# Performance work log

Measured on AMD Instinct MI355X. Metric: run time of the kernel, lower is better.

Reference implementation:

```python
import jax, jax.numpy as jnp
import numpy as np

B, L, D_MODEL = 2, 4096, 1024
D_STATE, D_CONV, EXPAND, HEADDIM = 128, 4, 2, 64
D_INNER = EXPAND * D_MODEL              # 2048
NHEADS = D_INNER // HEADDIM             # 32
CONV_DIM = D_INNER + 2 * D_STATE        # 2304 (ngroups=1)
D_IN_PROJ = 2 * D_INNER + 2 * D_STATE + NHEADS  # 4384
CHUNK = 128
EPS = 1e-5


def _segsum(a):
    # a: (..., T) log-decays -> (..., T, T) lower-triangular segment sums, -inf above diagonal
    T = a.shape[-1]
    cs = jnp.cumsum(a, axis=-1)
    seg = cs[..., :, None] - cs[..., None, :]
    mask = jnp.tril(jnp.ones((T, T), dtype=bool))
    return jnp.where(mask, seg, -jnp.inf)


def _forward(x, norm_w, norm_b, in_proj_w, conv_w, conv_b, dt_bias, A_log, D, rms_w, out_proj_w):
    b, l, _ = x.shape
    # pre-LayerNorm
    mu = jnp.mean(x, -1, keepdims=True)
    var = jnp.mean(jnp.square(x - mu), -1, keepdims=True)
    xn = (x - mu) * jax.lax.rsqrt(var + EPS) * norm_w + norm_b
    zxbcdt = xn @ in_proj_w.T                              # (b,l,D_IN_PROJ)
    z = zxbcdt[..., :D_INNER]
    xBC = zxbcdt[..., D_INNER:D_INNER + CONV_DIM]
    dt = jax.nn.softplus(zxbcdt[..., -NHEADS:] + dt_bias)  # (b,l,h)
    # causal depthwise conv1d + SiLU over (x, B, C)
    xc = jnp.pad(xBC.transpose(0, 2, 1), ((0, 0), (0, 0), (D_CONV - 1, 0)))
    xc = jax.lax.conv_general_dilated(xc, conv_w[:, None, :], (1,), 'VALID',
                                      feature_group_count=CONV_DIM,
                                      dimension_numbers=('NCH', 'OIH', 'NCH'))
    xBC = jax.nn.silu(xc + conv_b[None, :, None]).transpose(0, 2, 1)
    xs = xBC[..., :D_INNER].reshape(b, l, NHEADS, HEADDIM)
    Bm = xBC[..., D_INNER:D_INNER + D_STATE]               # (b,l,n)
    Cm = xBC[..., D_INNER + D_STATE:]                      # (b,l,n)
    # SSD chunked selective scan
    A = -jnp.exp(A_log)                                    # (h,)
    a = dt * A                                             # (b,l,h) log decay
    X = xs * dt[..., None]                                 # (b,l,h,p)
    c = l // CHUNK
    a_c = a.reshape(b, c, CHUNK, NHEADS).transpose(0, 3, 1, 2)   # (b,h,c,s)
    a_cum = jnp.cumsum(a_c, -1)
    Lmat = jnp.exp(_segsum(a_c))                           # (b,h,c,s,s)
    Xc = X.reshape(b, c, CHUNK, NHEADS, HEADDIM)
    Bc = Bm.reshape(b, c, CHUNK, D_STATE)
    Cc = Cm.reshape(b, c, CHUNK, D_STATE)
    # intra-chunk (diagonal block) output
    Y_diag = jnp.einsum('bcln,bcsn,bhcls,bcshp->bclhp', Cc, Bc, Lmat, Xc)
    # chunk-final states
    decay_states = jnp.exp(a_cum[..., -1:] - a_cum)        # (b,h,c,s)
    states = jnp.einsum('bcln,bhcl,bclhp->bchpn', Bc, decay_states, Xc)
    states = jnp.concatenate([jnp.zeros_like(states[:, :1]), states], axis=1)
    chunk_decay = jnp.exp(_segsum(jnp.pad(a_cum[..., -1], ((0, 0), (0, 0), (1, 0)))))  # (b,h,c+1,c+1)
    prev = jnp.einsum('bhzc,bchpn->bzhpn', chunk_decay, states)[:, :-1]  # (b,c,h,p,n)
    # inter-chunk (off-diagonal) output
    Y_off = jnp.einsum('bcln,bchpn,bhcl->bclhp', Cc, prev, jnp.exp(a_cum))
    y = (Y_diag + Y_off).reshape(b, l, NHEADS, HEADDIM) + D[None, None, :, None] * xs
    y = y.reshape(b, l, D_INNER)
    # gated RMSNorm (norm_before_gate=False): norm(y * silu(z))
    y = y * jax.nn.silu(z)
    y = y * jax.lax.rsqrt(jnp.mean(jnp.square(y), -1, keepdims=True) + EPS) * rms_w
    return x + y @ out_proj_w.T


def setup_inputs() -> dict:
    key = jax.random.key(0)
    ks = jax.random.split(key, 8)
    return {
        'x': jax.random.normal(ks[0], (B, L, D_MODEL), jnp.float32),
        'norm_w': jnp.ones((D_MODEL,), jnp.float32),
        'norm_b': jnp.zeros((D_MODEL,), jnp.float32),
        'in_proj_w': 0.02 * jax.random.normal(ks[1], (D_IN_PROJ, D_MODEL), jnp.float32),
        'conv_w': 0.2 * jax.random.normal(ks[2], (CONV_DIM, D_CONV), jnp.float32),
        'conv_b': jnp.zeros((CONV_DIM,), jnp.float32),
        'dt_bias': jax.random.uniform(ks[3], (NHEADS,), jnp.float32, -4.0, 0.0),
        'A_log': jnp.log(jax.random.uniform(ks[4], (NHEADS,), jnp.float32, 1.0, 16.0)),
        'D': jnp.ones((NHEADS,), jnp.float32),
        'rms_w': jnp.ones((D_INNER,), jnp.float32),
        'out_proj_w': 0.02 * jax.random.normal(ks[5], (D_MODEL, D_INNER), jnp.float32),
    }


def reference(x, norm_w, norm_b, in_proj_w, conv_w, conv_b, dt_bias, A_log, D, rms_w, out_proj_w):
    return _forward(x, norm_w, norm_b, in_proj_w, conv_w, conv_b, dt_bias, A_log, D, rms_w, out_proj_w)
```

## Files before the change

### kernel.cpp

```cpp
#include <hip/hip_runtime.h>

#define B_ 2
#define L_ 4096
#define DMODEL 1024
#define DSTATE 128
#define DINNER 2048
#define NH 32
#define HD 64
#define DPROJ 4384
#define DPROJP 4480
#define NC 32
#define EPSF 1e-5f
#define ROWS (B_*L_)

typedef unsigned short u16;
typedef __attribute__((ext_vector_type(8))) short s8v;
typedef __attribute__((ext_vector_type(4))) float f4v;
typedef __attribute__((ext_vector_type(4))) int i4v;
typedef __attribute__((ext_vector_type(2))) int i2v;
typedef __attribute__((ext_vector_type(4))) float fl4;

static __device__ __forceinline__ float b2f(u16 u){
  unsigned int x = ((unsigned int)u) << 16;
  return __builtin_bit_cast(float, x);
}
static __device__ __forceinline__ u16 f2b(float f){
  unsigned int x = __builtin_bit_cast(unsigned int, f);
  unsigned int r = x + 0x7FFFu + ((x >> 16) & 1u);
  return (u16)(r >> 16);
}
static __device__ __forceinline__ float softplusf(float x){
  return (x > 20.f) ? x : log1pf(expf(x));
}
static __device__ __forceinline__ void gl_lds16(const u16* g, u16* l){
  __builtin_amdgcn_global_load_lds(
    (const __attribute__((address_space(1))) unsigned int*)g,
    (__attribute__((address_space(3))) unsigned int*)l, 16, 0, 0);
}
static __device__ __forceinline__ int swz(int row, int col){
  return row*128 + ((((col >> 3) ^ (row & 15)) << 3) | (col & 7));
}
static __device__ __forceinline__ int swz64(int row, int col){
  return row*64 + ((((col >> 3) ^ (row & 7)) << 3) | (col & 7));
}
static __device__ __forceinline__ int osw(int t, int j){
  return t*64 + ((((j >> 3) ^ ((t >> 3) & 7)) << 3) | (j & 7));
}

__global__ void k_dbg(float* out, float v){ out[0] = v; }

#define NW1 ((size_t)DPROJP*DMODEL)
#define NW2 ((size_t)DMODEL*DINNER)
__global__ __launch_bounds__(256) void k_pack(const float* __restrict__ W1, const float* __restrict__ W2,
                                              u16* __restrict__ W1b, u16* __restrict__ W2b){
  size_t i = (size_t)blockIdx.x*256 + threadIdx.x;
  if (i < NW1){
    size_t n = i / DMODEL;
    W1b[i] = (n < DPROJ) ? f2b(W1[i]) : (u16)0;
  } else if (i < NW1 + NW2){
    size_t j = i - NW1;
    W2b[j] = f2b(W2[j]);
  }
}

__global__ __launch_bounds__(256) void k_ln(const float* __restrict__ x, const float* __restrict__ nw,
                                            const float* __restrict__ nb, u16* __restrict__ xn){
  int m = blockIdx.x; int tid = threadIdx.x;
  const float* row = x + (size_t)m*DMODEL;
  fl4 v = *(const fl4*)&row[tid*4];
  float s1 = v[0]+v[1]+v[2]+v[3];
  float s2 = v[0]*v[0]+v[1]*v[1]+v[2]*v[2]+v[3]*v[3];
  #pragma unroll
  for (int o=32;o;o>>=1){ s1 += __shfl_down(s1,o); s2 += __shfl_down(s2,o); }
  __shared__ float r1[4], r2[4];
  if ((tid&63)==0){ r1[tid>>6]=s1; r2[tid>>6]=s2; }
  __syncthreads();
  s1 = r1[0]+r1[1]+r1[2]+r1[3]; s2 = r2[0]+r2[1]+r2[2]+r2[3];
  float mu = s1 * (1.f/DMODEL);
  float var = s2 * (1.f/DMODEL) - mu*mu;
  float rs = rsqrtf(var + EPSF);
  u16* o = xn + (size_t)m*DMODEL + tid*4;
  #pragma unroll
  for (int k=0;k<4;k++)
    o[k] = f2b((v[k]-mu)*rs*nw[tid*4+k] + nb[tid*4+k]);
}

__global__ __launch_bounds__(256) void k_gemm_in(const u16* __restrict__ A, const u16* __restrict__ Bw,
                  u16* __restrict__ Cout, int K, int lda, int ldb, int ldc){
  __shared__ u16 smem[2*128*64];
  u16* sA = smem;
  u16* sB = smem + 128*64;
  int tid = threadIdx.x;
  int ln = tid & 63, wid = tid >> 6;
  int wr = wid >> 1, wc = wid & 1;
  size_t m0 = (size_t)blockIdx.x * 128, n0 = (size_t)blockIdx.y * 128;
  int lrow = ln >> 3;
  f4v acc[4][4] = {};
  for (int k0 = 0; k0 < K; k0 += 64){
    #pragma unroll
    for (int i = 0; i < 4; ++i){
      int seg = wid*4 + i;
      int row = seg*8 + lrow;
      int scol = ((ln & 7) ^ (row & 7)) * 8;
      gl_lds16(&A [(m0+row)*lda + k0 + scol], &sA[seg*512]);
      gl_lds16(&Bw[(n0+row)*ldb + k0 + scol], &sB[seg*512]);
    }
    __syncthreads();
    #pragma unroll
    for (int kk=0; kk<2; kk++){
      s8v af[4], bfr[4];
      #pragma unroll
      for (int t=0;t<4;t++){
        int col = kk*32 + (ln>>4)*8;
        af[t]  = *(const s8v*)&sA[swz64(wr*64+t*16+(ln&15), col)];
        bfr[t] = *(const s8v*)&sB[swz64(wc*64+t*16+(ln&15), col)];
      }
      #pragma unroll
      for (int mt=0;mt<4;mt++)
        #pragma unroll
        for (int nt=0;nt<4;nt++)
          acc[mt][nt] = __builtin_amdgcn_mfma_f32_16x16x32_bf16(af[mt], bfr[nt], acc[mt][nt], 0,0,0);
    }
    __syncthreads();
  }
  #pragma unroll
  for (int mt=0;mt<4;mt++)
    #pragma unroll
    for (int nt=0;nt<4;nt++)
      #pragma unroll
      for (int j=0;j<4;j++){
        int m = wr*64 + mt*16 + (ln>>4)*4 + j;
        int n = wc*64 + nt*16 + (ln&15);
        smem[m*128 + n] = f2b(acc[mt][nt][j]);
      }
  __syncthreads();
  #pragma unroll
  for (int it = 0; it < 8; ++it){
    int idx = (tid + it*256)*8;
    int row = idx >> 7, col = idx & 127;
    *(i4v*)&Cout[(m0+row)*ldc + n0 + col] = *(const i4v*)&smem[idx];
  }
}

__global__ __launch_bounds__(256) void k_gemm_out(const u16* __restrict__ A, const u16* __restrict__ Bw,
                  float* __restrict__ Cout, const float* __restrict__ resid,
                  int K, int lda, int ldb, int ldc){
  __shared__ u16 sA[128*64];
  __shared__ u16 sB[128*64];
  int tid = threadIdx.x;
  int ln = tid & 63, wid = tid >> 6;
  int wr = wid >> 1, wc = wid & 1;
  size_t m0 = (size_t)blockIdx.x * 128, n0 = (size_t)blockIdx.y * 128;
  int lrow = ln >> 3;
  f4v acc[4][4] = {};
  for (int k0 = 0; k0 < K; k0 += 64){
    #pragma unroll
    for (int i = 0; i < 4; ++i){
      int seg = wid*4 + i;
      int row = seg*8 + lrow;
      int scol = ((ln & 7) ^ (row & 7)) * 8;
      gl_lds16(&A [(m0+row)*lda + k0 + scol], &sA[seg*512]);
      gl_lds16(&Bw[(n0+row)*ldb + k0 + scol], &sB[seg*512]);
    }
    __syncthreads();
    #pragma unroll
    for (int kk=0; kk<2; kk++){
      s8v af[4], bfr[4];
      #pragma unroll
      for (int t=0;t<4;t++){
        int col = kk*32 + (ln>>4)*8;
        af[t]  = *(const s8v*)&sA[swz64(wr*64+t*16+(ln&15), col)];
        bfr[t] = *(const s8v*)&sB[swz64(wc*64+t*16+(ln&15), col)];
      }
      #pragma unroll
      for (int mt=0;mt<4;mt++)
        #pragma unroll
        for (int nt=0;nt<4;nt++)
          acc[mt][nt] = __builtin_amdgcn_mfma_f32_16x16x32_bf16(af[mt], bfr[nt], acc[mt][nt], 0,0,0);
    }
    __syncthreads();
  }
  #pragma unroll
  for (int mt=0;mt<4;mt++)
    #pragma unroll
    for (int nt=0;nt<4;nt++)
      #pragma unroll
      for (int j=0;j<4;j++){
        size_t m = m0 + wr*64 + mt*16 + (ln>>4)*4 + j;
        size_t n = n0 + wc*64 + nt*16 + (ln&15);
        Cout[m*ldc + n] = acc[mt][nt][j] + resid[m*ldc + n];
      }
}

__global__ __launch_bounds__(256) void k_conv(const u16* __restrict__ zx, const float* __restrict__ cw,
    const float* __restrict__ cb, const float* __restrict__ dtb, const float* __restrict__ A_log,
    u16* __restrict__ Xt, u16* __restrict__ Bln, u16* __restrict__ Bt,
    u16* __restrict__ Cln, float* __restrict__ dtg, float* __restrict__ acum){
  __shared__ u16 in_s[131*64];
  __shared__ u16 out_s[128*64];
  __shared__ float dt_s[128];
  __shared__ float a_s[128];
  int bid = blockIdx.x;
  int g = bid % 36;
  int c = (bid / 36) & 31;
  int b = bid / (36*32);
  int tid = threadIdx.x;
  int t0 = c*128;
  size_t rowb = (size_t)b*L_ + t0;
  for (int i8 = tid; i8 < 1048; i8 += 256){
    int r = i8 >> 3, j0 = (i8 & 7)*8;
    int t = t0 - 3 + r;
    i4v v;
    if (t >= 0) v = *(const i4v*)&zx[((size_t)b*L_ + t)*DPROJP + 2048 + g*64 + j0];
    else { v[0]=0; v[1]=0; v[2]=0; v[3]=0; }
    *(i4v*)&in_s[r*64 + j0] = v;
  }
  if (tid < 128){
    if (g < 32){
      float raw = b2f(zx[(rowb + tid)*DPROJP + (DPROJ - NH) + g]);
      float d = softplusf(raw + dtb[g]);
      dt_s[tid] = d;
      dtg[(size_t)(b*NH + g)*L_ + t0 + tid] = d;
      a_s[tid] = d * (-expf(A_log[g]));
    } else {
      dt_s[tid] = 0.f;
      a_s[tid] = 0.f;
    }
  }
  __syncthreads();
  #pragma unroll
  for (int d = 1; d < 128; d <<= 1){
    float v = 0.f;
    if (tid < 128 && tid >= d) v = a_s[tid - d];
    __syncthreads();
    if (tid < 128) a_s[tid] += v;
    __syncthreads();
  }
  if (g < 32 && tid < 128)
    acum[((size_t)((b*NH + g)*NC + c))*128 + tid] = a_s[tid];
  {
    int j = tid & 63;
    int ch = g*64 + j;
    float w0 = cw[ch*4+0], w1 = cw[ch*4+1], w2 = cw[ch*4+2], w3 = cw[ch*4+3];
    float bia = cb[ch];
    int tb = tid >> 6;
    #pragma unroll
    for (int it = 0; it < 32; ++it){
      int t = tb + it*4;
      float a = bia
        + w0*b2f(in_s[(t+0)*64 + j]) + w1*b2f(in_s[(t+1)*64 + j])
        + w2*b2f(in_s[(t+2)*64 + j]) + w3*b2f(in_s[(t+3)*64 + j]);
      out_s[osw(t, j)] = f2b(a / (1.f + __expf(-a)));
    }
  }
  __syncthreads();
  if (g < 32){
    for (int i = tid; i < 1024; i += 256){
      int j = i >> 4, tb = (i & 15)*8;
      i4v o; u16* ou = (u16*)&o;
      #pragma unroll
      for (int k = 0; k < 8; ++k)
        ou[k] = f2b(b2f(out_s[osw(tb + k, j)]) * dt_s[tb + k]);
      *(i4v*)&Xt[((size_t)((b*NH + g)*HD + j))*L_ + t0 + tb] = o;
    }
  } else {
    int q = g - 32;
    for (int i = tid; i < 1024; i += 256){
      int t = i >> 3, j0 = (i & 7)*8;
      i4v v = *(const i4v*)&out_s[osw(t, j0)];
      if (q < 2) *(i4v*)&Bln[(rowb + t)*DSTATE + q*64 + j0] = v;
      else       *(i4v*)&Cln[(rowb + t)*DSTATE + (q-2)*64 + j0] = v;
    }
    if (q < 2){
      for (int i = tid; i < 1024; i += 256){
        int j = i >> 4, tb = (i & 15)*8;
        i4v o; u16* ou = (u16*)&o;
        #pragma unroll
        for (int k = 0; k < 8; ++k) ou[k] = out_s[osw(tb + k, j)];
        *(i4v*)&Bt[((size_t)(b*DSTATE + q*64 + j))*L_ + t0 + tb] = o;
      }
    }
  }
}

__global__ __launch_bounds__(256) void k_states(const u16* __restrict__ Xt, const u16* __restrict__ Bt,
    const float* __restrict__ acum, u16* __restrict__ states){
  __shared__ u16 sX[64*128];
  __shared__ u16 sB[128*128];
  __shared__ float dec[128];
  int bid = blockIdx.x;
  int hg = bid & 7, c = (bid >> 3) & 31, b = bid >> 8;
  int tid = threadIdx.x;
  int ln = tid & 63, wid = tid >> 6;
  int wr = wid >> 1, wc = wid & 1;
  const u16* btb = Bt + (size_t)(b*DSTATE)*L_ + c*128;
  for (int i = tid*8; i < 128*128; i += 256*8){
    int n = i >> 7, l0 = i & 127;
    *(i4v*)&sB[swz(n, l0)] = *(const i4v*)&btb[(size_t)n*L_ + l0];
  }
  for (int hh = 0; hh < 4; ++hh){
    int h = hg*4 + hh;
    const float* acg = acum + ((size_t)((b*NH + h)*NC + c))*128;
    if (tid < 128) dec[tid] = __expf(acg[127] - acg[tid]);
    __syncthreads();
    const u16* xtb = Xt + ((size_t)((b*NH + h)*HD))*L_ + c*128;
    for (int i = tid*8; i < 64*128; i += 256*8){
      int p = i >> 7, l0 = i & 127;
      i4v v = *(const i4v*)&xtb[(size_t)p*L_ + l0];
      const u16* vu = (const u16*)&v;
      i4v o; u16* ou = (u16*)&o;
      #pragma unroll
      for (int j = 0; j < 8; ++j) ou[j] = f2b(b2f(vu[j]) * dec[l0 + j]);
      *(i4v*)&sX[swz(p, l0)] = o;
    }
    __syncthreads();
    f4v acc[2][4] = {};
    #pragma unroll
    for (int kk = 0; kk < 4; ++kk){
      s8v af[2], bfr[4];
      int col = kk*32 + (ln>>4)*8;
      #pragma unroll
      for (int t = 0; t < 2; ++t)
        af[t] = *(const s8v*)&sX[swz(wr*32 + t*16 + (ln&15), col)];
      #pragma unroll
      for (int t = 0; t < 4; ++t)
        bfr[t] = *(const s8v*)&sB[swz(wc*64 + t*16 + (ln&15), col)];
      #pragma unroll
      for (int mt = 0; mt < 2; ++mt)
        #pragma unroll
        for (int nt = 0; nt < 4; ++nt)
          acc[mt][nt] = __builtin_amdgcn_mfma_f32_16x16x32_bf16(af[mt], bfr[nt], acc[mt][nt], 0,0,0);
    }
    u16* out = states + ((size_t)((b*NC + c)*NH + h))*(HD*DSTATE);
    #pragma unroll
    for (int mt = 0; mt < 2; ++mt)
      #pragma unroll
      for (int nt = 0; nt < 4; ++nt){
        int n = wc*64 + nt*16 + (ln&15);
        #pragma unroll
        for (int j = 0; j < 4; ++j){
          int p = wr*32 + mt*16 + (ln>>4)*4 + j;
          out[(size_t)p*DSTATE + n] = f2b(acc[mt][nt][j]);
        }
      }
  }
}

__global__ __launch_bounds__(256) void k_scan(u16* __restrict__ states, const float* __restrict__ acum){
  int bid = blockIdx.x;
  int eb = bid & 7;
  int hb = bid >> 3;
  int h = hb & 31, b = hb >> 5;
  int tid = threadIdx.x;
  size_t ebase = (size_t)eb*1024 + (size_t)tid*4;
  size_t hoff = ((size_t)(b*NC*NH + h))*(HD*DSTATE) + ebase;
  float dec[NC];
  #pragma unroll
  for (int c = 0; c < NC; ++c)
    dec[c] = __expf(acum[((size_t)((b*NH + h)*NC + c))*128 + 127]);
  i2v w[NC];
  #pragma unroll
  for (int c = 0; c < NC; ++c)
    w[c] = *(const i2v*)&states[(size_t)c*(NH*HD*DSTATE) + hoff];
  float run[4] = {0.f, 0.f, 0.f, 0.f};
  #pragma unroll
  for (int c = 0; c < NC; ++c){
    u16* wu = (u16*)&w[c];
    #pragma unroll
    for (int j = 0; j < 4; ++j){
      float tmp = b2f(wu[j]);
      wu[j] = f2b(run[j]);
      run[j] = run[j]*dec[c] + tmp;
    }
  }
  #pragma unroll
  for (int c = 0; c < NC; ++c)
    *(i2v*)&states[(size_t)c*(NH*HD*DSTATE) + hoff] = w[c];
}

__global__ __launch_bounds__(256) void k_y(const u16* __restrict__ Cln, const u16* __restrict__ Bln,
    const u16* __restrict__ Xt, const u16* __restrict__ prev, const float* __restrict__ acum,
    const float* __restrict__ dtg, const float* __restrict__ Dp, u16* __restrict__ Y){
  __shared__ u16 sC[128*128];
  __shared__ u16 sBS[128*128];
  __shared__ float dt_s[128];
  int bid = blockIdx.x;
  int h = bid & 31, c = (bid >> 5) & 31, b = bid >> 10;
  int tid = threadIdx.x;
  size_t rowb = (size_t)b*L_ + c*128;
  const float* acg = acum + ((size_t)((b*NH + h)*NC + c))*128;
  if (tid < 128) dt_s[tid] = dtg[(size_t)(b*NH + h)*L_ + c*128 + tid];
  for (int i = tid*8; i < 128*128; i += 256*8){
    int row = i >> 7, col = i & 127;
    int d = swz(row, col);
    *(i4v*)&sC[d]  = *(const i4v*)&Cln[(rowb + row)*DSTATE + col];
    *(i4v*)&sBS[d] = *(const i4v*)&Bln[(rowb + row)*DSTATE + col];
  }
  __syncthreads();
  int ln = tid & 63, wid = tid >> 6;
  int wr = wid >> 1, wc = wid & 1;
  float Dh = Dp[h];
  f4v aS[4][4] = {};
  #pragma unroll
  for (int kk = 0; kk < 4; ++kk){
    s8v af[4], bfr[4];
    #pragma unroll
    for (int t = 0; t < 4; ++t){
      int col = kk*32 + (ln>>4)*8;
      af[t]  = *(const s8v*)&sC [swz(wr*64 + t*16 + (ln&15), col)];
      bfr[t] = *(const s8v*)&sBS[swz(wc*64 + t*16 + (ln&15), col)];
    }
    #pragma unroll
    for (int mt = 0; mt < 4; ++mt)
      #pragma unroll
      for (int nt = 0; nt < 4; ++nt)
        aS[mt][nt] = __builtin_amdgcn_mfma_f32_16x16x32_bf16(af[mt], bfr[nt], aS[mt][nt], 0,0,0);
  }
  __syncthreads();
  #pragma unroll
  for (int mt = 0; mt < 4; ++mt)
    #pragma unroll
    for (int nt = 0; nt < 4; ++nt){
      int s = wc*64 + nt*16 + (ln&15);
      float as = acg[s];
      #pragma unroll
      for (int j = 0; j < 4; ++j){
        int l = wr*64 + mt*16 + (ln>>4)*4 + j;
        float v = 0.f;
        if (s <= l){
          v = aS[mt][nt][j] * __expf(acg[l] - as);
          if (s == l) v += Dh / dt_s[l];
        }
        sBS[swz(l, s)] = f2b(v);
      }
    }
  __syncthreads();
  const u16* xtb = Xt + ((size_t)((b*NH + h)*HD))*L_ + c*128;
  const u16* pv = prev + ((size_t)((b*NC + c)*NH + h))*(HD*DSTATE);
  f4v aD[4][2] = {}, aO[4][2] = {};
  #pragma unroll
  for (int kk = 0; kk < 4; ++kk){
    s8v aSf[4], aCf[4], bXf[2], bPf[2];
    #pragma unroll
    for (int t = 0; t < 4; ++t){
      int col = kk*32 + (ln>>4)*8;
      int row = wr*64 + t*16 + (ln&15);
      aSf[t] = *(const s8v*)&sBS[swz(row, col)];
      aCf[t] = *(const s8v*)&sC[swz(row, col)];
    }
    #pragma unroll
    for (int t = 0; t < 2; ++t){
      int p = wc*32 + t*16 + (ln&15);
      int ko = kk*32 + (ln>>4)*8;
      bXf[t] = *(const s8v*)&xtb[(size_t)p*L_ + ko];
      bPf[t] = *(const s8v*)&pv[(size_t)p*DSTATE + ko];
    }
    #pragma unroll
    for (int mt = 0; mt < 4; ++mt)
      #pragma unroll
      for (int nt = 0; nt < 2; ++nt){
        aD[mt][nt] = __builtin_amdgcn_mfma_f32_16x16x32_bf16(aSf[mt], bXf[nt], aD[mt][nt], 0,0,0);
        aO[mt][nt] = __builtin_amdgcn_mfma_f32_16x16x32_bf16(aCf[mt], bPf[nt], aO[mt][nt], 0,0,0);
      }
  }
  __syncthreads();
  #pragma unroll
  for (int mt = 0; mt < 4; ++mt)
    #pragma unroll
    for (int nt = 0; nt < 2; ++nt){
      int p = wc*32 + nt*16 + (ln&15);
      #pragma unroll
      for (int j = 0; j < 4; ++j){
        int l = wr*64 + mt*16 + (ln>>4)*4 + j;
        float ex = __expf(acg[l]);
        float yv = aD[mt][nt][j] + ex*aO[mt][nt][j];
        sC[l*64 + (p ^ ((l & 7) << 3))] = f2b(yv);
      }
    }
  __syncthreads();
  #pragma unroll
  for (int it = 0; it < 4; ++it){
    int idx = (tid + it*256)*8;
    int row = idx >> 6, col0 = idx & 63;
    i4v v = *(const i4v*)&sC[row*64 + (col0 ^ ((row & 7) << 3))];
    *(i4v*)&Y[(rowb + row)*DINNER + h*HD + col0] = v;
  }
}

__global__ __launch_bounds__(256) void k_gate(u16* __restrict__ Y, const u16* __restrict__ zx,
                                              const float* __restrict__ rw){
  size_t m = blockIdx.x; int tid = threadIdx.x;
  u16* yrow = Y + m*DINNER + tid*8;
  const u16* zrow = zx + m*DPROJP + tid*8;
  i4v yv = *(const i4v*)yrow;
  i4v zv = *(const i4v*)zrow;
  const u16* yu = (const u16*)&yv;
  const u16* zu = (const u16*)&zv;
  float yg[8]; float ss = 0.f;
  #pragma unroll
  for (int k = 0; k < 8; ++k){
    float z = b2f(zu[k]);
    float g = z / (1.f + __expf(-z));
    float v = b2f(yu[k]) * g;
    yg[k] = v; ss += v*v;
  }
  #pragma unroll
  for (int o = 32; o; o >>= 1) ss += __shfl_down(ss, o);
  __shared__ float r[4];
  if ((tid&63) == 0) r[tid>>6] = ss;
  __syncthreads();
  ss = r[0]+r[1]+r[2]+r[3];
  float rstd = rsqrtf(ss*(1.f/DINNER) + EPSF);
  #pragma unroll
  for (int k = 0; k < 8; ++k)
    yrow[k] = f2b(yg[k]*rstd*rw[tid*8+k]);
}

extern "C" void kernel_launch(void* const* d_in, const int* in_sizes, int n_in,
                              void* d_out, int out_size, void* d_ws, size_t ws_size,
                              hipStream_t stream){
  const float* x        = (const float*)d_in[0];
  const float* norm_w   = (const float*)d_in[1];
  const float* norm_b   = (const float*)d_in[2];
  const float* in_proj  = (const float*)d_in[3];
  const float* conv_w   = (const float*)d_in[4];
  const float* conv_b   = (const float*)d_in[5];
  const float* dt_bias  = (const float*)d_in[6];
  const float* A_log    = (const float*)d_in[7];
  const float* Dp       = (const float*)d_in[8];
  const float* rms_w    = (const float*)d_in[9];
  const float* out_proj = (const float*)d_in[10];

  char* ws = (char*)d_ws;
  size_t off = 0;
  auto alloc = [&](size_t bytes) -> void* {
    void* p = ws + off;
    off += (bytes + 255) & ~(size_t)255;
    return p;
  };
  u16*   w1b    = (u16*)  alloc((size_t)DPROJP*DMODEL*2);
  u16*   w2b    = (u16*)  alloc((size_t)DMODEL*DINNER*2);
  u16*   xn     = (u16*)  alloc((size_t)ROWS*DMODEL*2);
  u16*   zx     = (u16*)  alloc((size_t)ROWS*DPROJP*2);
  u16*   Xt     = (u16*)  alloc((size_t)B_*NH*HD*L_*2);
  u16*   Bln    = (u16*)  alloc((size_t)ROWS*DSTATE*2);
  u16*   Bt     = (u16*)  alloc((size_t)B_*DSTATE*L_*2);
  u16*   Cln    = (u16*)  alloc((size_t)ROWS*DSTATE*2);
  float* dtg    = (float*)alloc((size_t)B_*NH*L_*4);
  float* acum   = (float*)alloc((size_t)B_*NH*NC*128*4);
  u16*   Y      = (u16*)  alloc((size_t)ROWS*DINNER*2);
  u16* states = (u16*)d_out;
  if (off > ws_size){
    k_dbg<<<1, 1, 0, stream>>>((float*)d_out, (float)ws_size);
    return;
  }

  k_pack<<<dim3((unsigned)((NW1 + NW2 + 255)/256)), 256, 0, stream>>>(in_proj, out_proj, w1b, w2b);
  k_ln<<<dim3(ROWS), 256, 0, stream>>>(x, norm_w, norm_b, xn);
  k_gemm_in<<<dim3(ROWS/128, DPROJP/128), 256, 0, stream>>>(xn, w1b, zx,
                                                            DMODEL, DMODEL, DMODEL, DPROJP);
  k_conv<<<dim3(B_*NC*36), 256, 0, stream>>>(zx, conv_w, conv_b, dt_bias, A_log,
                                             Xt, Bln, Bt, Cln, dtg, acum);
  k_states<<<dim3(B_*NC*(NH/4)), 256, 0, stream>>>(Xt, Bt, acum, states);
  k_scan<<<dim3(B_*NH*8), 256, 0, stream>>>(states, acum);
  k_y<<<dim3(B_*NC*NH), 256, 0, stream>>>(Cln, Bln, Xt, states, acum, dtg, Dp, Y);
  k_gate<<<dim3(ROWS), 256, 0, stream>>>(Y, zx, rms_w);
  k_gemm_out<<<dim3(ROWS/128, DMODEL/128), 256, 0, stream>>>(Y, w2b, (float*)d_out, x,
                                                             DINNER, DINNER, DINNER, DMODEL);
}
```

Before: 302.3 us.

## Fuse SiLU gating into k_y and fold RMSNorm into out-proj GEMM

```diff
diff --git a/kernel.cpp b/kernel.cpp
--- a/kernel.cpp
+++ b/kernel.cpp
@@ -52,6 +52,7 @@
 #define NW1 ((size_t)DPROJP*DMODEL)
 #define NW2 ((size_t)DMODEL*DINNER)
 __global__ __launch_bounds__(256) void k_pack(const float* __restrict__ W1, const float* __restrict__ W2,
+                                              const float* __restrict__ rw,
                                               u16* __restrict__ W1b, u16* __restrict__ W2b){
   size_t i = (size_t)blockIdx.x*256 + threadIdx.x;
   if (i < NW1){
@@ -59,7 +60,7 @@
     W1b[i] = (n < DPROJ) ? f2b(W1[i]) : (u16)0;
   } else if (i < NW1 + NW2){
     size_t j = i - NW1;
-    W2b[j] = f2b(W2[j]);
+    W2b[j] = f2b(W2[j] * rw[j & (DINNER - 1)]);
   }
 }
 
@@ -144,6 +145,7 @@
 
 __global__ __launch_bounds__(256) void k_gemm_out(const u16* __restrict__ A, const u16* __restrict__ Bw,
                   float* __restrict__ Cout, const float* __restrict__ resid,
+                  const float* __restrict__ rstd,
                   int K, int lda, int ldb, int ldc){
   __shared__ u16 sA[128*64];
   __shared__ u16 sB[128*64];
@@ -188,7 +190,7 @@
       for (int j=0;j<4;j++){
         size_t m = m0 + wr*64 + mt*16 + (ln>>4)*4 + j;
         size_t n = n0 + wc*64 + nt*16 + (ln&15);
-        Cout[m*ldc + n] = acc[mt][nt][j] + resid[m*ldc + n];
+        Cout[m*ldc + n] = acc[mt][nt][j]*rstd[m] + resid[m*ldc + n];
       }
 }
 
@@ -380,16 +382,35 @@
 
 __global__ __launch_bounds__(256) void k_y(const u16* __restrict__ Cln, const u16* __restrict__ Bln,
     const u16* __restrict__ Xt, const u16* __restrict__ prev, const float* __restrict__ acum,
-    const float* __restrict__ dtg, const float* __restrict__ Dp, u16* __restrict__ Y){
+    const float* __restrict__ dtg, const float* __restrict__ Dp, const u16* __restrict__ zx,
+    u16* __restrict__ Y, float* __restrict__ part){
   __shared__ u16 sC[128*128];
   __shared__ u16 sBS[128*128];
   __shared__ float dt_s[128];
+  __shared__ float ac_s[128];
   int bid = blockIdx.x;
   int h = bid & 31, c = (bid >> 5) & 31, b = bid >> 10;
   int tid = threadIdx.x;
   size_t rowb = (size_t)b*L_ + c*128;
   const float* acg = acum + ((size_t)((b*NH + h)*NC + c))*128;
-  if (tid < 128) dt_s[tid] = dtg[(size_t)(b*NH + h)*L_ + c*128 + tid];
+  if (tid < 128){
+    dt_s[tid] = dtg[(size_t)(b*NH + h)*L_ + c*128 + tid];
+    ac_s[tid] = acg[tid];
+  }
+  int ln = tid & 63, wid = tid >> 6;
+  int wr = wid >> 1, wc = wid & 1;
+  const u16* xtb = Xt + ((size_t)((b*NH + h)*HD))*L_ + c*128;
+  const u16* pv = prev + ((size_t)((b*NC + c)*NH + h))*(HD*DSTATE);
+  s8v bXf[4][2], bPf[4][2];
+  #pragma unroll
+  for (int kk = 0; kk < 4; ++kk)
+    #pragma unroll
+    for (int t = 0; t < 2; ++t){
+      int p = wc*32 + t*16 + (ln&15);
+      int ko = kk*32 + (ln>>4)*8;
+      bXf[kk][t] = *(const s8v*)&xtb[(size_t)p*L_ + ko];
+      bPf[kk][t] = *(const s8v*)&pv[(size_t)p*DSTATE + ko];
+    }
   for (int i = tid*8; i < 128*128; i += 256*8){
     int row = i >> 7, col = i & 127;
     int d = swz(row, col);
@@ -397,8 +418,6 @@
     *(i4v*)&sBS[d] = *(const i4v*)&Bln[(rowb + row)*DSTATE + col];
   }
   __syncthreads();
-  int ln = tid & 63, wid = tid >> 6;
-  int wr = wid >> 1, wc = wid & 1;
   float Dh = Dp[h];
   f4v aS[4][4] = {};
   #pragma unroll
@@ -422,25 +441,23 @@
     #pragma unroll
     for (int nt = 0; nt < 4; ++nt){
       int s = wc*64 + nt*16 + (ln&15);
-      float as = acg[s];
+      float as = ac_s[s];
       #pragma unroll
       for (int j = 0; j < 4; ++j){
         int l = wr*64 + mt*16 + (ln>>4)*4 + j;
         float v = 0.f;
         if (s <= l){
-          v = aS[mt][nt][j] * __expf(acg[l] - as);
+          v = aS[mt][nt][j] * __expf(ac_s[l] - as);
           if (s == l) v += Dh / dt_s[l];
         }
         sBS[swz(l, s)] = f2b(v);
       }
     }
   __syncthreads();
-  const u16* xtb = Xt + ((size_t)((b*NH + h)*HD))*L_ + c*128;
-  const u16* pv = prev + ((size_t)((b*NC + c)*NH + h))*(HD*DSTATE);
   f4v aD[4][2] = {}, aO[4][2] = {};
   #pragma unroll
   for (int kk = 0; kk < 4; ++kk){
-    s8v aSf[4], aCf[4], bXf[2], bPf[2];
+    s8v aSf[4], aCf[4];
     #pragma unroll
     for (int t = 0; t < 4; ++t){
       int col = kk*32 + (ln>>4)*8;
@@ -449,18 +466,11 @@
       aCf[t] = *(const s8v*)&sC[swz(row, col)];
     }
     #pragma unroll
-    for (int t = 0; t < 2; ++t){
-      int p = wc*32 + t*16 + (ln&15);
-      int ko = kk*32 + (ln>>4)*8;
-      bXf[t] = *(const s8v*)&xtb[(size_t)p*L_ + ko];
-      bPf[t] = *(const s8v*)&pv[(size_t)p*DSTATE + ko];
-    }
-    #pragma unroll
     for (int mt = 0; mt < 4; ++mt)
       #pragma unroll
       for (int nt = 0; nt < 2; ++nt){
-        aD[mt][nt] = __builtin_amdgcn_mfma_f32_16x16x32_bf16(aSf[mt], bXf[nt], aD[mt][nt], 0,0,0);
-        aO[mt][nt] = __builtin_amdgcn_mfma_f32_16x16x32_bf16(aCf[mt], bPf[nt], aO[mt][nt], 0,0,0);
+        aD[mt][nt] = __builtin_amdgcn_mfma_f32_16x16x32_bf16(aSf[mt], bXf[kk][nt], aD[mt][nt], 0,0,0);
+        aO[mt][nt] = __builtin_amdgcn_mfma_f32_16x16x32_bf16(aCf[mt], bPf[kk][nt], aO[mt][nt], 0,0,0);
       }
   }
   __syncthreads();
@@ -472,7 +482,7 @@
       #pragma unroll
       for (int j = 0; j < 4; ++j){
         int l = wr*64 + mt*16 + (ln>>4)*4 + j;
-        float ex = __expf(acg[l]);
+        float ex = __expf(ac_s[l]);
         float yv = aD[mt][nt][j] + ex*aO[mt][nt][j];
         sC[l*64 + (p ^ ((l & 7) << 3))] = f2b(yv);
       }
@@ -482,38 +492,38 @@
   for (int it = 0; it < 4; ++it){
     int idx = (tid + it*256)*8;
     int row = idx >> 6, col0 = idx & 63;
-    i4v v = *(const i4v*)&sC[row*64 + (col0 ^ ((row & 7) << 3))];
-    *(i4v*)&Y[(rowb + row)*DINNER + h*HD + col0] = v;
-  }
-}
-
-__global__ __launch_bounds__(256) void k_gate(u16* __restrict__ Y, const u16* __restrict__ zx,
-                                              const float* __restrict__ rw){
-  size_t m = blockIdx.x; int tid = threadIdx.x;
-  u16* yrow = Y + m*DINNER + tid*8;
-  const u16* zrow = zx + m*DPROJP + tid*8;
-  i4v yv = *(const i4v*)yrow;
-  i4v zv = *(const i4v*)zrow;
-  const u16* yu = (const u16*)&yv;
-  const u16* zu = (const u16*)&zv;
-  float yg[8]; float ss = 0.f;
-  #pragma unroll
-  for (int k = 0; k < 8; ++k){
-    float z = b2f(zu[k]);
-    float g = z / (1.f + __expf(-z));
-    float v = b2f(yu[k]) * g;
-    yg[k] = v; ss += v*v;
-  }
-  #pragma unroll
-  for (int o = 32; o; o >>= 1) ss += __shfl_down(ss, o);
-  __shared__ float r[4];
-  if ((tid&63) == 0) r[tid>>6] = ss;
-  __syncthreads();
-  ss = r[0]+r[1]+r[2]+r[3];
-  float rstd = rsqrtf(ss*(1.f/DINNER) + EPSF);
-  #pragma unroll
-  for (int k = 0; k < 8; ++k)
-    yrow[k] = f2b(yg[k]*rstd*rw[tid*8+k]);
+    i4v yv = *(const i4v*)&sC[row*64 + (col0 ^ ((row & 7) << 3))];
+    i4v zv = *(const i4v*)&zx[(rowb + row)*DPROJP + h*HD + col0];
+    const u16* yu = (const u16*)&yv;
+    const u16* zu = (const u16*)&zv;
+    i4v o; u16* ou = (u16*)&o;
+    float ss = 0.f;
+    #pragma unroll
+    for (int k = 0; k < 8; ++k){
+      float z = b2f(zu[k]);
+      float g = z / (1.f + __expf(-z));
+      float v = b2f(yu[k]) * g;
+      ou[k] = f2b(v);
+      ss += v*v;
+    }
+    *(i4v*)&Y[(rowb + row)*DINNER + h*HD + col0] = o;
+    ss += __shfl_xor(ss, 1);
+    ss += __shfl_xor(ss, 2);
+    ss += __shfl_xor(ss, 4);
+    if ((tid & 7) == 0) part[(rowb + row)*NH + h] = ss;
+  }
+}
+
+__global__ __launch_bounds__(256) void k_rstd(const float* __restrict__ part, float* __restrict__ rstd){
+  int m = blockIdx.x*256 + threadIdx.x;
+  const fl4* p = (const fl4*)&part[(size_t)m*NH];
+  float s = 0.f;
+  #pragma unroll
+  for (int q = 0; q < NH/4; ++q){
+    fl4 v = p[q];
+    s += v[0]+v[1]+v[2]+v[3];
+  }
+  rstd[m] = rsqrtf(s*(1.f/DINNER) + EPSF);
 }
 
 extern "C" void kernel_launch(void* const* d_in, const int* in_sizes, int n_in,
@@ -549,13 +559,15 @@
   float* dtg    = (float*)alloc((size_t)B_*NH*L_*4);
   float* acum   = (float*)alloc((size_t)B_*NH*NC*128*4);
   u16*   Y      = (u16*)  alloc((size_t)ROWS*DINNER*2);
+  float* part   = (float*)alloc((size_t)ROWS*NH*4);
+  float* rstd   = (float*)alloc((size_t)ROWS*4);
   u16* states = (u16*)d_out;
   if (off > ws_size){
     k_dbg<<<1, 1, 0, stream>>>((float*)d_out, (float)ws_size);
     return;
   }
 
-  k_pack<<<dim3((unsigned)((NW1 + NW2 + 255)/256)), 256, 0, stream>>>(in_proj, out_proj, w1b, w2b);
+  k_pack<<<dim3((unsigned)((NW1 + NW2 + 255)/256)), 256, 0, stream>>>(in_proj, out_proj, rms_w, w1b, w2b);
   k_ln<<<dim3(ROWS), 256, 0, stream>>>(x, norm_w, norm_b, xn);
   k_gemm_in<<<dim3(ROWS/128, DPROJP/128), 256, 0, stream>>>(xn, w1b, zx,
                                                             DMODEL, DMODEL, DMODEL, DPROJP);
@@ -563,8 +575,8 @@
                                              Xt, Bln, Bt, Cln, dtg, acum);
   k_states<<<dim3(B_*NC*(NH/4)), 256, 0, stream>>>(Xt, Bt, acum, states);
   k_scan<<<dim3(B_*NH*8), 256, 0, stream>>>(states, acum);
-  k_y<<<dim3(B_*NC*NH), 256, 0, stream>>>(Cln, Bln, Xt, states, acum, dtg, Dp, Y);
-  k_gate<<<dim3(ROWS), 256, 0, stream>>>(Y, zx, rms_w);
-  k_gemm_out<<<dim3(ROWS/128, DMODEL/128), 256, 0, stream>>>(Y, w2b, (float*)d_out, x,
+  k_y<<<dim3(B_*NC*NH), 256, 0, stream>>>(Cln, Bln, Xt, states, acum, dtg, Dp, zx, Y, part);
+  k_rstd<<<dim3(ROWS/256), 256, 0, stream>>>(part, rstd);
+  k_gemm_out<<<dim3(ROWS/128, DMODEL/128), 256, 0, stream>>>(Y, w2b, (float*)d_out, x, rstd,
                                                              DINNER, DINNER, DINNER, DMODEL);
 }
```

Result: slower. 336.9 us (+11.5%).

## Shrink k_y shared memory by staging B in halves and reusing C buffer

Applied to the files above, without the earlier changes.

```diff
diff --git a/kernel.cpp b/kernel.cpp
--- a/kernel.cpp
+++ b/kernel.cpp
@@ -382,7 +382,7 @@
     const u16* __restrict__ Xt, const u16* __restrict__ prev, const float* __restrict__ acum,
     const float* __restrict__ dtg, const float* __restrict__ Dp, u16* __restrict__ Y){
   __shared__ u16 sC[128*128];
-  __shared__ u16 sBS[128*128];
+  __shared__ u16 sBh[128*64];
   __shared__ float dt_s[128];
   int bid = blockIdx.x;
   int h = bid & 31, c = (bid >> 5) & 31, b = bid >> 10;
@@ -392,9 +392,11 @@
   if (tid < 128) dt_s[tid] = dtg[(size_t)(b*NH + h)*L_ + c*128 + tid];
   for (int i = tid*8; i < 128*128; i += 256*8){
     int row = i >> 7, col = i & 127;
-    int d = swz(row, col);
-    *(i4v*)&sC[d]  = *(const i4v*)&Cln[(rowb + row)*DSTATE + col];
-    *(i4v*)&sBS[d] = *(const i4v*)&Bln[(rowb + row)*DSTATE + col];
+    *(i4v*)&sC[swz(row, col)] = *(const i4v*)&Cln[(rowb + row)*DSTATE + col];
+  }
+  for (int i = tid*8; i < 128*64; i += 256*8){
+    int row = i >> 6, col = i & 63;
+    *(i4v*)&sBh[swz64(row, col)] = *(const i4v*)&Bln[(rowb + row)*DSTATE + col];
   }
   __syncthreads();
   int ln = tid & 63, wid = tid >> 6;
@@ -402,19 +404,60 @@
   float Dh = Dp[h];
   f4v aS[4][4] = {};
   #pragma unroll
-  for (int kk = 0; kk < 4; ++kk){
+  for (int kk = 0; kk < 2; ++kk){
     s8v af[4], bfr[4];
+    int col = kk*32 + (ln>>4)*8;
     #pragma unroll
     for (int t = 0; t < 4; ++t){
-      int col = kk*32 + (ln>>4)*8;
       af[t]  = *(const s8v*)&sC [swz(wr*64 + t*16 + (ln&15), col)];
-      bfr[t] = *(const s8v*)&sBS[swz(wc*64 + t*16 + (ln&15), col)];
+      bfr[t] = *(const s8v*)&sBh[swz64(wc*64 + t*16 + (ln&15), col)];
     }
     #pragma unroll
     for (int mt = 0; mt < 4; ++mt)
       #pragma unroll
       for (int nt = 0; nt < 4; ++nt)
         aS[mt][nt] = __builtin_amdgcn_mfma_f32_16x16x32_bf16(af[mt], bfr[nt], aS[mt][nt], 0,0,0);
+  }
+  __syncthreads();
+  for (int i = tid*8; i < 128*64; i += 256*8){
+    int row = i >> 6, col = i & 63;
+    *(i4v*)&sBh[swz64(row, col)] = *(const i4v*)&Bln[(rowb + row)*DSTATE + 64 + col];
+  }
+  __syncthreads();
+  #pragma unroll
+  for (int kk = 0; kk < 2; ++kk){
+    s8v af[4], bfr[4];
+    int colh = kk*32 + (ln>>4)*8;
+    #pragma unroll
+    for (int t = 0; t < 4; ++t){
+      af[t]  = *(const s8v*)&sC [swz(wr*64 + t*16 + (ln&15), 64 + colh)];
+      bfr[t] = *(const s8v*)&sBh[swz64(wc*64 + t*16 + (ln&15), colh)];
+    }
+    #pragma unroll
+    for (int mt = 0; mt < 4; ++mt)
+      #pragma unroll
+      for (int nt = 0; nt < 4; ++nt)
+        aS[mt][nt] = __builtin_amdgcn_mfma_f32_16x16x32_bf16(af[mt], bfr[nt], aS[mt][nt], 0,0,0);
+  }
+  const u16* pv = prev + ((size_t)((b*NC + c)*NH + h))*(HD*DSTATE);
+  f4v aO[4][2] = {};
+  #pragma unroll
+  for (int kk = 0; kk < 4; ++kk){
+    s8v aCf[4], bPf[2];
+    int col = kk*32 + (ln>>4)*8;
+    #pragma unroll
+    for (int t = 0; t < 4; ++t)
+      aCf[t] = *(const s8v*)&sC[swz(wr*64 + t*16 + (ln&15), col)];
+    #pragma unroll
+    for (int t = 0; t < 2; ++t){
+      int p = wc*32 + t*16 + (ln&15);
+      bPf[t] = *(const s8v*)&pv[(size_t)p*DSTATE + col];
+    }
+    #pragma unroll
+    for (int mt = 0; mt < 4; ++mt)
+      #pragma unroll
+      for (int nt = 0; nt < 2; ++nt)
+        aO[mt][nt] = __builtin_amdgcn_mfma_f32_16x16x32_bf16(aCf[mt], bPf[nt], aO[mt][nt], 0,0,0);
   }
   __syncthreads();
   #pragma unroll
@@ -431,37 +474,29 @@
           v = aS[mt][nt][j] * __expf(acg[l] - as);
           if (s == l) v += Dh / dt_s[l];
         }
-        sBS[swz(l, s)] = f2b(v);
+        sC[swz(l, s)] = f2b(v);
       }
     }
   __syncthreads();
   const u16* xtb = Xt + ((size_t)((b*NH + h)*HD))*L_ + c*128;
-  const u16* pv = prev + ((size_t)((b*NC + c)*NH + h))*(HD*DSTATE);
-  f4v aD[4][2] = {}, aO[4][2] = {};
+  f4v aD[4][2] = {};
   #pragma unroll
   for (int kk = 0; kk < 4; ++kk){
-    s8v aSf[4], aCf[4], bXf[2], bPf[2];
-    #pragma unroll
-    for (int t = 0; t < 4; ++t){
-      int col = kk*32 + (ln>>4)*8;
-      int row = wr*64 + t*16 + (ln&15);
-      aSf[t] = *(const s8v*)&sBS[swz(row, col)];
-      aCf[t] = *(const s8v*)&sC[swz(row, col)];
-    }
+    s8v aSf[4], bXf[2];
+    int col = kk*32 + (ln>>4)*8;
+    #pragma unroll
+    for (int t = 0; t < 4; ++t)
+      aSf[t] = *(const s8v*)&sC[swz(wr*64 + t*16 + (ln&15), col)];
     #pragma unroll
     for (int t = 0; t < 2; ++t){
       int p = wc*32 + t*16 + (ln&15);
-      int ko = kk*32 + (ln>>4)*8;
-      bXf[t] = *(const s8v*)&xtb[(size_t)p*L_ + ko];
-      bPf[t] = *(const s8v*)&pv[(size_t)p*DSTATE + ko];
+      bXf[t] = *(const s8v*)&xtb[(size_t)p*L_ + col];
     }
     #pragma unroll
     for (int mt = 0; mt < 4; ++mt)
       #pragma unroll
-      for (int nt = 0; nt < 2; ++nt){
+      for (int nt = 0; nt < 2; ++nt)
         aD[mt][nt] = __builtin_amdgcn_mfma_f32_16x16x32_bf16(aSf[mt], bXf[nt], aD[mt][nt], 0,0,0);
-        aO[mt][nt] = __builtin_amdgcn_mfma_f32_16x16x32_bf16(aCf[mt], bPf[nt], aO[mt][nt], 0,0,0);
-      }
   }
   __syncthreads();
   #pragma unroll
@@ -474,7 +509,7 @@
         int l = wr*64 + mt*16 + (ln>>4)*4 + j;
         float ex = __expf(acg[l]);
         float yv = aD[mt][nt][j] + ex*aO[mt][nt][j];
-        sC[l*64 + (p ^ ((l & 7) << 3))] = f2b(yv);
+        sBh[l*64 + (p ^ ((l & 7) << 3))] = f2b(yv);
       }
     }
   __syncthreads();
@@ -482,7 +517,7 @@
   for (int it = 0; it < 4; ++it){
     int idx = (tid + it*256)*8;
     int row = idx >> 6, col0 = idx & 63;
-    i4v v = *(const i4v*)&sC[row*64 + (col0 ^ ((row & 7) << 3))];
+    i4v v = *(const i4v*)&sBh[row*64 + (col0 ^ ((row & 7) << 3))];
     *(i4v*)&Y[(rowb + row)*DINNER + h*HD + col0] = v;
   }
 }
```

New measurement: 303.6 us. No clear change (+0.4%).
